# Optimization experiments

Hardware: AMD Instinct MI355X
Metric: run time of the kernel (lower is better)

Reference implementation:

```python
import jax, jax.numpy as jnp
import numpy as np

B, C, F, T = 8, 2, 64, 1024
E = C * F            # embed_dim = 128
H = 8                # num_heads
DH = E // H          # head_dim = 16


def setup_inputs() -> dict:
    key = jax.random.key(0)
    ks = jax.random.split(key, 14)
    s = 0.05  # small init scale for numerical stability
    return {
        "x_re": jax.random.normal(ks[0], (B, C, F, T), jnp.float32),
        "x_im": jax.random.normal(ks[1], (B, C, F, T), jnp.float32),
        "win_re": jax.random.normal(ks[2], (3 * E, E), jnp.float32) * s,
        "win_im": jax.random.normal(ks[3], (3 * E, E), jnp.float32) * s,
        "bin_re": jax.random.normal(ks[4], (3 * E,), jnp.float32) * s,
        "bin_im": jax.random.normal(ks[5], (3 * E,), jnp.float32) * s,
        "wout_re": jax.random.normal(ks[6], (E, E), jnp.float32) * s,
        "wout_im": jax.random.normal(ks[7], (E, E), jnp.float32) * s,
        "bout_re": jax.random.normal(ks[8], (E,), jnp.float32) * s,
        "bout_im": jax.random.normal(ks[9], (E,), jnp.float32) * s,
        "wt_re": jax.random.normal(ks[10], (E, E), jnp.float32) * s,
        "wt_im": jax.random.normal(ks[11], (E, E), jnp.float32) * s,
        "bt_re": jax.random.normal(ks[12], (E,), jnp.float32) * s,
        "bt_im": jax.random.normal(ks[13], (E,), jnp.float32) * s,
    }


def _forward(x_re, x_im, win_re, win_im, bin_re, bin_im,
             wout_re, wout_im, bout_re, bout_im,
             wt_re, wt_im, bt_re, bt_im):
    cplx = lambda r, i: (r + 1j * i).astype(jnp.complex64)
    x = cplx(x_re, x_im)                 # [B,C,F,T]
    win, bin_ = cplx(win_re, win_im), cplx(bin_re, bin_im)
    wout, bout = cplx(wout_re, wout_im), cplx(bout_re, bout_im)
    wt, bt = cplx(wt_re, wt_im), cplx(bt_re, bt_im)

    # flatten(1,2).transpose(1,2): [B,C,F,T] -> [B,E,T] -> [B,T,E]
    xs = jnp.transpose(x.reshape(B, E, T), (0, 2, 1))

    # packed complex qkv projection
    qkv = xs @ win.T + bin_              # [B,T,3E]
    q, k, v = jnp.split(qkv, 3, axis=-1)
    split_heads = lambda t: jnp.transpose(t.reshape(B, T, H, DH), (0, 2, 1, 3))
    q, k, v = split_heads(q), split_heads(k), split_heads(v)  # [B,H,T,DH]

    # complex attention scores Q K^H; softmax over real part
    scores = jnp.einsum("bhqd,bhkd->bhqk", q, jnp.conj(k)) * (DH ** -0.5)
    attn = jax.nn.softmax(scores.real, axis=-1).astype(jnp.complex64)
    o = jnp.einsum("bhqk,bhkd->bhqd", attn, v)               # [B,H,T,DH]
    o = jnp.transpose(o, (0, 2, 1, 3)).reshape(B, T, E)
    o = o @ wout.T + bout                # attention out-proj

    # transform: complex Linear E -> E
    y = o @ wt.T + bt                    # [B,T,E]

    # unflatten(-1,(C,F)) then movedim(1,-1): [B,T,C,F] -> [B,C,F,T]
    y = jnp.moveaxis(y.reshape(B, T, C, F), 1, -1)
    return jnp.stack([y.real, y.imag], axis=0)  # [2,B,C,F,T]


def reference(x_re, x_im, win_re, win_im, bin_re, bin_im,
              wout_re, wout_im, bout_re, bout_im,
              wt_re, wt_im, bt_re, bt_im):
    return _forward(x_re, x_im, win_re, win_im, bin_re, bin_im,
                    wout_re, wout_im, bout_re, bout_im,
                    wt_re, wt_im, bt_re, bt_im)
```

## Files before the change

### kernel.cpp

```cpp
#include <hip/hip_runtime.h>
#include <hip/hip_bf16.h>

#define B 8
#define T 1024
#define E 128
#define H 8
#define DH 16
#define E3 384

typedef __attribute__((ext_vector_type(8))) short short8;
typedef __attribute__((ext_vector_type(4))) short short4s;
typedef __attribute__((ext_vector_type(4))) float f32x4;

static __device__ inline short bf16s(float x) {
    union { float f; unsigned u; } v; v.f = x;
    unsigned r = v.u + 0x7fffu + ((v.u >> 16) & 1u);
    return (short)(r >> 16);
}

#if __has_builtin(__builtin_amdgcn_exp2f)
static __device__ inline float fexp2(float x) { return __builtin_amdgcn_exp2f(x); }
#else
static __device__ inline float fexp2(float x) { return __builtin_exp2f(x); }
#endif

static __device__ inline __hip_bfloat162 pk2(float a, float b) {
    float2 t; t.x = a; t.y = b;
    return __float22bfloat162_rn(t);
}

static __device__ inline void stage16(const void* g, void* l) {
    __builtin_amdgcn_global_load_lds(
        (const __attribute__((address_space(1))) void*)g,
        (__attribute__((address_space(3))) void*)l,
        16, 0, 0);
}

#define QSCALE 0.36067376022224085f

__global__ void pack_win_kernel(
    const float* __restrict__ win_re, const float* __restrict__ win_im,
    short* __restrict__ Wp_re, short* __restrict__ Wp_im)
{
    int idx = blockIdx.x * 256 + threadIdx.x;
    int j = idx >> 7, e = idx & 127;
    float wr = win_re[idx], wi = win_im[idx];
    Wp_re[j*256 + e]       = bf16s(wr);
    Wp_re[j*256 + 128 + e] = bf16s(-wi);
    Wp_im[j*256 + e]       = bf16s(wi);
    Wp_im[j*256 + 128 + e] = bf16s(wr);
}

__global__ __launch_bounds__(256, 2) void qkv_fuse_kernel(
    const float* __restrict__ x_re, const float* __restrict__ x_im,
    const short* __restrict__ Wp_re, const short* __restrict__ Wp_im,
    const float* __restrict__ bin_re, const float* __restrict__ bin_im,
    const float* __restrict__ wout_re, const float* __restrict__ wout_im,
    const float* __restrict__ bout_re, const float* __restrict__ bout_im,
    const float* __restrict__ wt_re,   const float* __restrict__ wt_im,
    const float* __restrict__ bt_re,   const float* __restrict__ bt_im,
    short* __restrict__ Qpk, short* __restrict__ Kpk,
    short* __restrict__ Vtre, short* __restrict__ Vtim,
    short* __restrict__ Wfp_re, short* __restrict__ Wfp_im,
    float* __restrict__ bf_re, float* __restrict__ bf_im)
{
    __shared__ short8 xsh[4][8][64];

    int bid = blockIdx.x;
    int tid = threadIdx.x;

    if (bid < 512) {
        int wave = tid >> 6, lane = tid & 63;
        int col  = lane & 15, quad = lane >> 4;
        int jg    = bid & 3;
        int ttile = bid >> 2;
        int b  = ttile >> 4;
        int t0 = (ttile & 15) * 64;

        {
            int tglob = t0 + wave*16 + col;
            #pragma unroll
            for (int kt = 0; kt < 8; ++kt) {
                const float* xs = (kt < 4) ? x_re : x_im;
                const float* p = &xs[((long)(b*E + (kt & 3)*32 + quad*8))*T + tglob];
                float v0 = p[0], v1 = p[(long)T], v2 = p[2L*T], v3 = p[3L*T];
                float v4 = p[4L*T], v5 = p[5L*T], v6 = p[6L*T], v7 = p[7L*T];
                short8 xv;
                __hip_bfloat162* xp = (__hip_bfloat162*)&xv;
                xp[0] = pk2(v0, v1); xp[1] = pk2(v2, v3);
                xp[2] = pk2(v4, v5); xp[3] = pk2(v6, v7);
                xsh[wave][kt][lane] = xv;
            }
        }
        __syncthreads();

        short8 xr[4][8];
        #pragma unroll
        for (int ts = 0; ts < 4; ++ts)
            #pragma unroll
            for (int kt = 0; kt < 8; ++kt)
                xr[ts][kt] = xsh[ts][kt][lane];

        const f32x4 zero = {0.f,0.f,0.f,0.f};

        for (int ui = 0; ui < 3; ++ui) {
            int idx  = wave * 3 + ui;
            int half = idx >= 6;
            int u    = half ? idx - 6 : idx;
            int jt   = jg * 6 + u;
            const short* Wsel = half ? Wp_im : Wp_re;
            const float* bias = half ? bin_im : bin_re;
            const short* wrow = &Wsel[(jt*16 + col)*256 + quad*8];

            f32x4 acc[4] = {zero, zero, zero, zero};
            #pragma unroll
            for (int kt = 0; kt < 8; ++kt) {
                short8 af = *(const short8*)(wrow + kt*32);
                #pragma unroll
                for (int ts = 0; ts < 4; ++ts)
                    acc[ts] = __builtin_amdgcn_mfma_f32_16x16x32_bf16(af, xr[ts][kt], acc[ts], 0, 0, 0);
            }

            int which = jt >> 3;
            int h = jt & 7;
            float scale = (which == 0) ? QSCALE : 1.0f;
            long bh = b*H + h;

            #pragma unroll
            for (int ts = 0; ts < 4; ++ts) {
                int tb = t0 + ts*16 + col;
                f32x4 res;
                #pragma unroll
                for (int r = 0; r < 4; ++r) {
                    int jgl = which*128 + h*16 + quad*4 + r;
                    res[r] = (acc[ts][r] + bias[jgl]) * scale;
                }
                if (which == 2) {
                    short* vt = half ? Vtim : Vtre;
                    int tloc = tb & 31, tblk = tb & ~31;
                    int u2 = tloc & 15;
                    int kk = (u2 >> 2)*8 + (u2 & 3) + ((tloc >= 16) ? 4 : 0);
                    #pragma unroll
                    for (int r = 0; r < 4; ++r)
                        vt[(bh*DH + quad*4 + r)*T + tblk + kk] = bf16s(res[r]);
                } else {
                    short* qk = (which == 0) ? Qpk : Kpk;
                    short4s pk;
                    __hip_bfloat162* pp = (__hip_bfloat162*)&pk;
                    pp[0] = pk2(res[0], res[1]);
                    pp[1] = pk2(res[2], res[3]);
                    *(short4s*)&qk[(bh*T + tb)*32 + half*16 + quad*4] = pk;
                }
            }
        }
    } else if (bid < 576) {
        int idx = (bid - 512) * 256 + tid;
        int j = idx >> 7, e = idx & 127;
        float ar = 0.f, ai = 0.f;
        for (int m = 0; m < E; ++m) {
            float tr = wt_re[j*E+m], ti = wt_im[j*E+m];
            float pr = wout_re[m*E+e], pi = wout_im[m*E+e];
            ar += tr*pr - ti*pi;
            ai += tr*pi + ti*pr;
        }
        Wfp_re[j*256 + e]       = bf16s(ar);
        Wfp_re[j*256 + 128 + e] = bf16s(-ai);
        Wfp_im[j*256 + e]       = bf16s(ai);
        Wfp_im[j*256 + 128 + e] = bf16s(ar);
    } else {
        if (tid < E) {
            float br = bt_re[tid], bi = bt_im[tid];
            for (int m = 0; m < E; ++m) {
                float tr = wt_re[tid*E+m], ti = wt_im[tid*E+m];
                br += tr*bout_re[m] - ti*bout_im[m];
                bi += tr*bout_im[m] + ti*bout_re[m];
            }
            bf_re[tid] = br; bf_im[tid] = bi;
        }
    }
}

__global__ __launch_bounds__(256, 2) void attn_mfma_kernel(
    const short* __restrict__ Qpk, const short* __restrict__ Kpk,
    const short* __restrict__ Vtre, const short* __restrict__ Vtim,
    short* __restrict__ Opk)
{
    __shared__ short lbuf[3][4][512];

    int id   = blockIdx.x;
    int bh   = id & 63;
    int q0   = (id >> 6) * 128;
    int tid  = threadIdx.x;
    int wave = tid >> 6;
    int lane = tid & 63;
    int col  = lane & 15;
    int quad = lane >> 4;

    long kq_base = (long)bh * T * 32;
    int qbase = q0 + wave * 32;

    short8 qfA = *(const short8*)&Qpk[kq_base + (long)(qbase + col)*32 + quad*8];
    short8 qfB = *(const short8*)&Qpk[kq_base + (long)(qbase + 16 + col)*32 + quad*8];

    const short* gsrc;
    int gstep;
    if (wave == 0)      { gsrc = &Kpk[kq_base + col*32 + quad*8];              gstep = 1024; }
    else if (wave == 1) { gsrc = &Kpk[kq_base + 512 + col*32 + quad*8];        gstep = 1024; }
    else if (wave == 2) { gsrc = &Vtre[(long)bh*DH*T + (long)col*T + quad*8];  gstep = 32; }
    else                { gsrc = &Vtim[(long)bh*DH*T + (long)col*T + quad*8];  gstep = 32; }

    short8 ones;
    #pragma unroll
    for (int i = 0; i < 8; ++i) ones[i] = (short)0x3F80;

    f32x4 oAr = {0,0,0,0}, oAi = {0,0,0,0}, lA = {0,0,0,0};
    f32x4 oBr = {0,0,0,0}, oBi = {0,0,0,0}, lB = {0,0,0,0};
    const f32x4 zero = {0.f,0.f,0.f,0.f};

    stage16(gsrc, &lbuf[0][wave][0]); gsrc += gstep;
    stage16(gsrc, &lbuf[1][wave][0]); gsrc += gstep;
    asm volatile("s_waitcnt vmcnt(1)" ::: "memory");
    __builtin_amdgcn_s_barrier();
    __builtin_amdgcn_sched_barrier(0);

    for (int i = 0; i < 32; ++i) {
        int cur = i % 3;
        int nxt = (i + 2) % 3;
        stage16(gsrc, &lbuf[nxt][wave][0]);
        gsrc += gstep;

        short8 kf0 = *(const short8*)&lbuf[cur][0][lane*8];
        short8 kf1 = *(const short8*)&lbuf[cur][1][lane*8];
        short8 vr  = *(const short8*)&lbuf[cur][2][lane*8];
        short8 vi  = *(const short8*)&lbuf[cur][3][lane*8];

        __builtin_amdgcn_s_setprio(1);
        f32x4 sA0 = __builtin_amdgcn_mfma_f32_16x16x32_bf16(kf0, qfA, zero, 0, 0, 0);
        f32x4 sA1 = __builtin_amdgcn_mfma_f32_16x16x32_bf16(kf1, qfA, zero, 0, 0, 0);
        f32x4 sB0 = __builtin_amdgcn_mfma_f32_16x16x32_bf16(kf0, qfB, zero, 0, 0, 0);
        f32x4 sB1 = __builtin_amdgcn_mfma_f32_16x16x32_bf16(kf1, qfB, zero, 0, 0, 0);
        __builtin_amdgcn_s_setprio(0);

        short8 pfA, pfB;
        {
            __hip_bfloat162* pa = (__hip_bfloat162*)&pfA;
            pa[0] = pk2(fexp2(sA0[0]), fexp2(sA0[1]));
            pa[1] = pk2(fexp2(sA0[2]), fexp2(sA0[3]));
            pa[2] = pk2(fexp2(sA1[0]), fexp2(sA1[1]));
            pa[3] = pk2(fexp2(sA1[2]), fexp2(sA1[3]));
            __hip_bfloat162* pb = (__hip_bfloat162*)&pfB;
            pb[0] = pk2(fexp2(sB0[0]), fexp2(sB0[1]));
            pb[1] = pk2(fexp2(sB0[2]), fexp2(sB0[3]));
            pb[2] = pk2(fexp2(sB1[0]), fexp2(sB1[1]));
            pb[3] = pk2(fexp2(sB1[2]), fexp2(sB1[3]));
        }

        __builtin_amdgcn_s_setprio(1);
        oAr = __builtin_amdgcn_mfma_f32_16x16x32_bf16(vr, pfA, oAr, 0, 0, 0);
        oAi = __builtin_amdgcn_mfma_f32_16x16x32_bf16(vi, pfA, oAi, 0, 0, 0);
        lA  = __builtin_amdgcn_mfma_f32_16x16x32_bf16(ones, pfA, lA, 0, 0, 0);
        oBr = __builtin_amdgcn_mfma_f32_16x16x32_bf16(vr, pfB, oBr, 0, 0, 0);
        oBi = __builtin_amdgcn_mfma_f32_16x16x32_bf16(vi, pfB, oBi, 0, 0, 0);
        lB  = __builtin_amdgcn_mfma_f32_16x16x32_bf16(ones, pfB, lB, 0, 0, 0);
        __builtin_amdgcn_s_setprio(0);

        asm volatile("s_waitcnt vmcnt(1)" ::: "memory");
        __builtin_amdgcn_s_barrier();
        __builtin_amdgcn_sched_barrier(0);
    }

    int b = bh >> 3, h = bh & 7;
    float invA = 1.0f / lA[0];
    float invB = 1.0f / lB[0];

    long orowA = ((long)(b*T + qbase + col))*256 + h*16 + quad*4;
    {
        short4s pr, pi_;
        __hip_bfloat162* a = (__hip_bfloat162*)&pr;
        a[0] = pk2(oAr[0]*invA, oAr[1]*invA);
        a[1] = pk2(oAr[2]*invA, oAr[3]*invA);
        __hip_bfloat162* c = (__hip_bfloat162*)&pi_;
        c[0] = pk2(oAi[0]*invA, oAi[1]*invA);
        c[1] = pk2(oAi[2]*invA, oAi[3]*invA);
        *(short4s*)&Opk[orowA]       = pr;
        *(short4s*)&Opk[orowA + 128] = pi_;
    }
    long orowB = orowA + 16L*256;
    {
        short4s pr, pi_;
        __hip_bfloat162* a = (__hip_bfloat162*)&pr;
        a[0] = pk2(oBr[0]*invB, oBr[1]*invB);
        a[1] = pk2(oBr[2]*invB, oBr[3]*invB);
        __hip_bfloat162* c = (__hip_bfloat162*)&pi_;
        c[0] = pk2(oBi[0]*invB, oBi[1]*invB);
        c[1] = pk2(oBi[2]*invB, oBi[3]*invB);
        *(short4s*)&Opk[orowB]       = pr;
        *(short4s*)&Opk[orowB + 128] = pi_;
    }
}

__global__ __launch_bounds__(256) void outproj_mfma_kernel(
    const short* __restrict__ Opk,
    const short* __restrict__ Wfp_re, const short* __restrict__ Wfp_im,
    const float* __restrict__ bf_re, const float* __restrict__ bf_im,
    float* __restrict__ out)
{
    int tid  = threadIdx.x;
    int wave = tid >> 6, lane = tid & 63;
    int col  = lane & 15, quad = lane >> 4;
    int ttile = blockIdx.x;
    int b  = ttile >> 6;
    int tb = (ttile & 63) * 16 + col;
    long trow = (long)b*T + tb;

    short8 xf[8];
    #pragma unroll
    for (int kt = 0; kt < 8; ++kt)
        xf[kt] = *(const short8*)&Opk[trow*256 + kt*32 + quad*8];

    const f32x4 zero = {0.f,0.f,0.f,0.f};
    #pragma unroll
    for (int ni = 0; ni < 4; ++ni) {
        int nt = wave * 4 + ni;
        int is_im = nt >= 8;
        int jt = is_im ? nt - 8 : nt;
        const short* Wsel = is_im ? Wfp_im : Wfp_re;
        const short* wrow = &Wsel[(jt*16 + col)*256 + quad*8];
        f32x4 acc = zero;
        #pragma unroll
        for (int kt = 0; kt < 8; ++kt) {
            short8 af = *(const short8*)(wrow + kt*32);
            acc = __builtin_amdgcn_mfma_f32_16x16x32_bf16(af, xf[kt], acc, 0, 0, 0);
        }
        const float* bias = is_im ? bf_im : bf_re;
        long part = is_im ? (long)B*E*T : 0;
        #pragma unroll
        for (int r = 0; r < 4; ++r) {
            int j = jt*16 + quad*4 + r;
            out[part + ((long)(b*E + j))*T + tb] = acc[r] + bias[j];
        }
    }
}

extern "C" void kernel_launch(void* const* d_in, const int* in_sizes, int n_in,
                              void* d_out, int out_size, void* d_ws, size_t ws_size,
                              hipStream_t stream)
{
    const float* x_re    = (const float*)d_in[0];
    const float* x_im    = (const float*)d_in[1];
    const float* win_re  = (const float*)d_in[2];
    const float* win_im  = (const float*)d_in[3];
    const float* bin_re  = (const float*)d_in[4];
    const float* bin_im  = (const float*)d_in[5];
    const float* wout_re = (const float*)d_in[6];
    const float* wout_im = (const float*)d_in[7];
    const float* bout_re = (const float*)d_in[8];
    const float* bout_im = (const float*)d_in[9];
    const float* wt_re   = (const float*)d_in[10];
    const float* wt_im   = (const float*)d_in[11];
    const float* bt_re   = (const float*)d_in[12];
    const float* bt_im   = (const float*)d_in[13];
    float* out = (float*)d_out;

    short* Qpk  = (short*)d_ws;
    short* Kpk  = Qpk + (long)B*H*T*32;
    short* Vtre = Kpk + (long)B*H*T*32;
    short* Vtim = Vtre + (long)B*H*DH*T;
    short* Opk  = Vtim + (long)B*H*DH*T;
    short* Wp_re  = Opk + (long)B*T*256;
    short* Wp_im  = Wp_re + E3*256;
    short* Wfp_re = Wp_im + E3*256;
    short* Wfp_im = Wfp_re + E*256;
    float* bf_re  = (float*)(Wfp_im + E*256);
    float* bf_im  = bf_re + E;

    pack_win_kernel<<<dim3(E3*E/256), dim3(256), 0, stream>>>(
        win_re, win_im, Wp_re, Wp_im);

    qkv_fuse_kernel<<<dim3(577), dim3(256), 0, stream>>>(
        x_re, x_im, Wp_re, Wp_im, bin_re, bin_im,
        wout_re, wout_im, bout_re, bout_im,
        wt_re, wt_im, bt_re, bt_im,
        Qpk, Kpk, Vtre, Vtim,
        Wfp_re, Wfp_im, bf_re, bf_im);

    attn_mfma_kernel<<<dim3(8 * 64), dim3(256), 0, stream>>>(
        Qpk, Kpk, Vtre, Vtim, Opk);

    outproj_mfma_kernel<<<dim3(512), dim3(256), 0, stream>>>(
        Opk, Wfp_re, Wfp_im, bf_re, bf_im, out);
}
```

Measured before the change: 135.7 us.

## Deepen attention K/V staging ring and retile out-projection for shared-memory activation reuse

The attention kernel moves from a 3-slot to a 6-slot LDS ring. It now stages two K/V tiles per iteration and processes two tiles between barriers, which halves barrier count and raises prefetch depth. The out-projection kernel is retiled so each block handles 64 timesteps across one group of 4 output tiles. Activations are staged once into shared memory and each weight fragment is reused across 4 time subtiles. The cost is more LDS and registers per block, with occupancy hinted at 2 blocks.

```diff
diff --git a/kernel.cpp b/kernel.cpp
--- a/kernel.cpp
+++ b/kernel.cpp
@@ -185,7 +185,7 @@
     const short* __restrict__ Vtre, const short* __restrict__ Vtim,
     short* __restrict__ Opk)
 {
-    __shared__ short lbuf[3][4][512];
+    __shared__ short lbuf[6][4][512];
 
     int id   = blockIdx.x;
     int bh   = id & 63;
@@ -217,22 +217,11 @@
     f32x4 oBr = {0,0,0,0}, oBi = {0,0,0,0}, lB = {0,0,0,0};
     const f32x4 zero = {0.f,0.f,0.f,0.f};
 
-    stage16(gsrc, &lbuf[0][wave][0]); gsrc += gstep;
-    stage16(gsrc, &lbuf[1][wave][0]); gsrc += gstep;
-    asm volatile("s_waitcnt vmcnt(1)" ::: "memory");
-    __builtin_amdgcn_s_barrier();
-    __builtin_amdgcn_sched_barrier(0);
-
-    for (int i = 0; i < 32; ++i) {
-        int cur = i % 3;
-        int nxt = (i + 2) % 3;
-        stage16(gsrc, &lbuf[nxt][wave][0]);
-        gsrc += gstep;
-
-        short8 kf0 = *(const short8*)&lbuf[cur][0][lane*8];
-        short8 kf1 = *(const short8*)&lbuf[cur][1][lane*8];
-        short8 vr  = *(const short8*)&lbuf[cur][2][lane*8];
-        short8 vi  = *(const short8*)&lbuf[cur][3][lane*8];
+    auto COMPUTE = [&](int bi) {
+        short8 kf0 = *(const short8*)&lbuf[bi][0][lane*8];
+        short8 kf1 = *(const short8*)&lbuf[bi][1][lane*8];
+        short8 vr  = *(const short8*)&lbuf[bi][2][lane*8];
+        short8 vi  = *(const short8*)&lbuf[bi][3][lane*8];
 
         __builtin_amdgcn_s_setprio(1);
         f32x4 sA0 = __builtin_amdgcn_mfma_f32_16x16x32_bf16(kf0, qfA, zero, 0, 0, 0);
@@ -263,11 +252,29 @@
         oBi = __builtin_amdgcn_mfma_f32_16x16x32_bf16(vi, pfB, oBi, 0, 0, 0);
         lB  = __builtin_amdgcn_mfma_f32_16x16x32_bf16(ones, pfB, lB, 0, 0, 0);
         __builtin_amdgcn_s_setprio(0);
-
-        asm volatile("s_waitcnt vmcnt(1)" ::: "memory");
+    };
+
+    stage16(gsrc, &lbuf[0][wave][0]); gsrc += gstep;
+    stage16(gsrc, &lbuf[1][wave][0]); gsrc += gstep;
+    stage16(gsrc, &lbuf[2][wave][0]); gsrc += gstep;
+    stage16(gsrc, &lbuf[3][wave][0]); gsrc += gstep;
+    asm volatile("s_waitcnt vmcnt(2)" ::: "memory");
+    __builtin_amdgcn_s_barrier();
+    __builtin_amdgcn_sched_barrier(0);
+
+    for (int i = 0; i < 32; i += 2) {
+        stage16(gsrc, &lbuf[(i+4)%6][wave][0]); gsrc += gstep;
+        stage16(gsrc, &lbuf[(i+5)%6][wave][0]); gsrc += gstep;
+
+        COMPUTE(i % 6);
+        COMPUTE((i+1) % 6);
+
+        asm volatile("s_waitcnt vmcnt(2)" ::: "memory");
         __builtin_amdgcn_s_barrier();
         __builtin_amdgcn_sched_barrier(0);
     }
+
+    asm volatile("s_waitcnt vmcnt(0)" ::: "memory");
 
     int b = bh >> 3, h = bh & 7;
     float invA = 1.0f / lA[0];
@@ -299,45 +306,63 @@
     }
 }
 
-__global__ __launch_bounds__(256) void outproj_mfma_kernel(
+__global__ __launch_bounds__(256, 2) void outproj_mfma_kernel(
     const short* __restrict__ Opk,
     const short* __restrict__ Wfp_re, const short* __restrict__ Wfp_im,
     const float* __restrict__ bf_re, const float* __restrict__ bf_im,
     float* __restrict__ out)
 {
+    __shared__ short8 osh[4][8][64];
+
     int tid  = threadIdx.x;
     int wave = tid >> 6, lane = tid & 63;
     int col  = lane & 15, quad = lane >> 4;
-    int ttile = blockIdx.x;
-    int b  = ttile >> 6;
-    int tb = (ttile & 63) * 16 + col;
-    long trow = (long)b*T + tb;
-
-    short8 xf[8];
+    int jg    = blockIdx.x & 3;
+    int ttile = blockIdx.x >> 2;
+    int b  = ttile >> 4;
+    int t0 = (ttile & 15) * 64;
+
+    {
+        long trow = (long)b*T + t0 + wave*16 + col;
+        #pragma unroll
+        for (int kt = 0; kt < 8; ++kt)
+            stage16(&Opk[trow*256 + kt*32 + quad*8], &osh[wave][kt][0]);
+    }
+    __syncthreads();
+
+    short8 xr[4][8];
     #pragma unroll
-    for (int kt = 0; kt < 8; ++kt)
-        xf[kt] = *(const short8*)&Opk[trow*256 + kt*32 + quad*8];
+    for (int ts = 0; ts < 4; ++ts)
+        #pragma unroll
+        for (int kt = 0; kt < 8; ++kt)
+            xr[ts][kt] = osh[ts][kt][lane];
 
     const f32x4 zero = {0.f,0.f,0.f,0.f};
+
+    int nt = jg*4 + wave;
+    int is_im = nt >= 8;
+    int jt = is_im ? nt - 8 : nt;
+    const short* Wsel = is_im ? Wfp_im : Wfp_re;
+    const short* wrow = &Wsel[(jt*16 + col)*256 + quad*8];
+
+    f32x4 acc[4] = {zero, zero, zero, zero};
     #pragma unroll
-    for (int ni = 0; ni < 4; ++ni) {
-        int nt = wave * 4 + ni;
-        int is_im = nt >= 8;
-        int jt = is_im ? nt - 8 : nt;
-        const short* Wsel = is_im ? Wfp_im : Wfp_re;
-        const short* wrow = &Wsel[(jt*16 + col)*256 + quad*8];
-        f32x4 acc = zero;
+    for (int kt = 0; kt < 8; ++kt) {
+        short8 af = *(const short8*)(wrow + kt*32);
         #pragma unroll
-        for (int kt = 0; kt < 8; ++kt) {
-            short8 af = *(const short8*)(wrow + kt*32);
-            acc = __builtin_amdgcn_mfma_f32_16x16x32_bf16(af, xf[kt], acc, 0, 0, 0);
-        }
-        const float* bias = is_im ? bf_im : bf_re;
-        long part = is_im ? (long)B*E*T : 0;
+        for (int ts = 0; ts < 4; ++ts)
+            acc[ts] = __builtin_amdgcn_mfma_f32_16x16x32_bf16(af, xr[ts][kt], acc[ts], 0, 0, 0);
+    }
+
+    const float* bias = is_im ? bf_im : bf_re;
+    long part = is_im ? (long)B*E*T : 0;
+    #pragma unroll
+    for (int ts = 0; ts < 4; ++ts) {
+        int tb = t0 + ts*16 + col;
         #pragma unroll
         for (int r = 0; r < 4; ++r) {
             int j = jt*16 + quad*4 + r;
-            out[part + ((long)(b*E + j))*T + tb] = acc[r] + bias[j];
+            out[part + ((long)(b*E + j))*T + tb] = acc[ts][r] + bias[j];
         }
     }
 }
```

After: 132.8 us, median of 2. -2.1%, faster.
